# Performance work log

Hardware: AMD Instinct MI355X
Metric: run time of the kernel (lower is better)

## Reference

```python
import jax, jax.numpy as jnp
import numpy as np

N_NODES = 50000
N_EDGES = 800000
FEAT_DIM = 64
NUM_RELS = 8


def setup_inputs() -> dict:
    key = jax.random.key(0)
    k1, k2, k3, k4, k5 = jax.random.split(key, 5)
    features = jax.random.normal(k1, (N_NODES, FEAT_DIM), dtype=jnp.float32)
    # xavier_uniform with relu gain ~= sqrt(2)*sqrt(6/(D+D))
    limit = np.sqrt(2.0) * np.sqrt(6.0 / (FEAT_DIM + FEAT_DIM))
    weight_r = jax.random.uniform(k2, (NUM_RELS, FEAT_DIM, FEAT_DIM), dtype=jnp.float32,
                                  minval=-limit, maxval=limit)
    src = jax.random.randint(k3, (N_EDGES,), 0, N_NODES, dtype=jnp.int64 if jax.config.jax_enable_x64 else jnp.int32)
    dst = jax.random.randint(k4, (N_EDGES,), 0, N_NODES, dtype=src.dtype)
    etype = jax.random.randint(k5, (N_EDGES,), 0, NUM_RELS, dtype=src.dtype)
    return {"features": features, "weight_r": weight_r, "src": src, "dst": dst, "etype": etype}


def reference(features, weight_r, src, dst, etype):
    N, D = features.shape
    c = 0.2
    # in-degree of each destination node (DGL 'deg' node data)
    deg = jax.ops.segment_sum(jnp.ones(dst.shape, dtype=features.dtype), dst, num_segments=N)
    # relation-batched matmul: h @ W_r for every relation, then gather per edge.
    # [R, N, D] = 8*50000*64 floats -- cheap vs. materializing [E, D, D] weights.
    hw = jnp.einsum('nd,rdf->rnf', features, weight_r)
    msg = hw[etype, src] / deg[dst][:, None]          # [E, D]
    M = jax.ops.segment_sum(msg, dst, num_segments=N)  # scatter-sum mailbox reduce
    updated = jax.nn.relu(c * features + (1.0 - c) * M)
    # DGL only applies reduce to nodes that received messages; others keep h.
    return jnp.where((deg > 0)[:, None], updated, features)
```

## Files before the change

kernel.cpp:

```cpp
#include <hip/hip_runtime.h>
#include <hip/hip_bf16.h>

#define N_NODES 50000
#define N_EDGES 800000
#define FEAT 64
#define NRELS 8
#define NBUCK 196
#define EPB 4096
#define NBP 196
#define BCAP 5120
#define FB_BLOCKS 782
#define NPB 32
#define FUSE_BLOCKS 1563

typedef __attribute__((ext_vector_type(8))) short bf16x8;
typedef __attribute__((ext_vector_type(4))) float f32x4;

static __host__ __device__ inline size_t align256(size_t x) { return (x + 255) & ~(size_t)255; }

__device__ inline unsigned short f2b(float f) {
    unsigned u = __builtin_bit_cast(unsigned, f);
    unsigned r = (u + 0x7fffu + ((u >> 16) & 1u)) >> 16;
    return (unsigned short)r;
}
__device__ inline float b2f(unsigned short u) {
    unsigned v = ((unsigned)u) << 16;
    return __builtin_bit_cast(float, v);
}

__global__ void bfill_kernel(const int* __restrict__ dst, const int* __restrict__ srcv,
                             const int* __restrict__ et, const float* __restrict__ W,
                             const float* __restrict__ feat,
                             int* __restrict__ bcnt, int* __restrict__ tmp,
                             unsigned short* __restrict__ WtT,
                             unsigned short* __restrict__ Fb, int E, int N) {
    const int t = threadIdx.x;

    if (blockIdx.x >= NBP) {
        const int fbb = blockIdx.x - NBP;
        if (fbb < 32) {
            int i4 = fbb * 256 + t;
            float4 v = ((const float4*)W)[i4];
            int bse = i4 * 4;
            int f0 = bse & 63;
            int rd = bse >> 6;
            int d  = rd & 63;
            int r  = rd >> 6;
            unsigned short* w0 = WtT + ((size_t)(r * 64 + f0) * 64 + d);
            w0[0 * 64] = f2b(v.x);
            w0[1 * 64] = f2b(v.y);
            w0[2 * 64] = f2b(v.z);
            w0[3 * 64] = f2b(v.w);
        }
        const int node = fbb * 64 + (t >> 2);
        if (node >= N) return;
        const int seg = t & 3;
        const float4* F4 = (const float4*)feat + (size_t)node * 16 + seg * 4;
        float4 v0 = F4[0], v1 = F4[1], v2 = F4[2], v3 = F4[3];
        bf16x8 b0, b1;
        b0[0] = (short)f2b(v0.x); b0[1] = (short)f2b(v0.y);
        b0[2] = (short)f2b(v0.z); b0[3] = (short)f2b(v0.w);
        b0[4] = (short)f2b(v1.x); b0[5] = (short)f2b(v1.y);
        b0[6] = (short)f2b(v1.z); b0[7] = (short)f2b(v1.w);
        b1[0] = (short)f2b(v2.x); b1[1] = (short)f2b(v2.y);
        b1[2] = (short)f2b(v2.z); b1[3] = (short)f2b(v2.w);
        b1[4] = (short)f2b(v3.x); b1[5] = (short)f2b(v3.y);
        b1[6] = (short)f2b(v3.z); b1[7] = (short)f2b(v3.w);
        *(bf16x8*)(Fb + (size_t)node * 64 + seg * 16)     = b0;
        *(bf16x8*)(Fb + (size_t)node * 64 + seg * 16 + 8) = b1;
        return;
    }

    __shared__ int hist[256];
    __shared__ int base[256];
    __shared__ int lcur[256];
    hist[t] = 0; lcur[t] = 0;
    __syncthreads();

    const int4* dst4 = (const int4*)dst;
    const int4* src4 = (const int4*)srcv;
    const int4* et4  = (const int4*)et;
    const int n4 = E >> 2;
    int bk[16], pk[16];
#pragma unroll
    for (int k = 0; k < 4; k++) {
        int i4 = blockIdx.x * 1024 + t + k * 256;
        if (i4 < n4) {
            int4 d = dst4[i4];
            int4 s = src4[i4];
            int4 r = et4[i4];
            const int dd[4] = {d.x, d.y, d.z, d.w};
            const int ss[4] = {s.x, s.y, s.z, s.w};
            const int rr[4] = {r.x, r.y, r.z, r.w};
#pragma unroll
            for (int j = 0; j < 4; j++) {
                int idx = k * 4 + j;
                bk[idx] = dd[j] >> 8;
                pk[idx] = (ss[j] & 0xFFFF) | (rr[j] << 16) | ((dd[j] & 255) << 19);
                atomicAdd(&hist[bk[idx]], 1);
            }
        } else {
#pragma unroll
            for (int j = 0; j < 4; j++) bk[k * 4 + j] = -1;
        }
    }
    __syncthreads();
    if (t < NBUCK && hist[t] > 0)
        base[t] = t * BCAP + atomicAdd(&bcnt[t], hist[t]);
    __syncthreads();
#pragma unroll
    for (int k = 0; k < 16; k++) {
        if (bk[k] >= 0) {
            int r = atomicAdd(&lcur[bk[k]], 1);
            int pos = base[bk[k]] + r;
            if (pos < (bk[k] + 1) * BCAP)
                tmp[pos] = pk[k];
        }
    }
}

__global__ void mid_kernel(const int* __restrict__ bcnt, const int* __restrict__ tmp,
                           int* __restrict__ spk, int* __restrict__ off_s,
                           int* __restrict__ off_e, int N) {
    __shared__ int hist[2048];
    __shared__ int s[256];
    const int t = threadIdx.x;

    const int b = blockIdx.x;
    const int n0 = b * 256;
    const int nn = min(256, N - n0);
    const int s0 = b * BCAP;
    const int s1 = s0 + min(bcnt[b], BCAP);

#pragma unroll
    for (int j = 0; j < 8; j++) hist[t * 8 + j] = 0;
    __syncthreads();
    for (int i = s0 + t; i < s1; i += 1024) {
        int v0 = tmp[i];
        int v1 = (i + 256 < s1) ? tmp[i + 256] : -1;
        int v2 = (i + 512 < s1) ? tmp[i + 512] : -1;
        int v3 = (i + 768 < s1) ? tmp[i + 768] : -1;
        atomicAdd(&hist[(v0 >> 16) & 0x7FF], 1);
        if (v1 >= 0) atomicAdd(&hist[(v1 >> 16) & 0x7FF], 1);
        if (v2 >= 0) atomicAdd(&hist[(v2 >> 16) & 0x7FF], 1);
        if (v3 >= 0) atomicAdd(&hist[(v3 >> 16) & 0x7FF], 1);
    }
    __syncthreads();
    int loc[8], st[8], T = 0;
#pragma unroll
    for (int j = 0; j < 8; j++) loc[j] = hist[t * 8 + j];
#pragma unroll
    for (int j = 0; j < 8; j++) { st[j] = T; T += loc[j]; }
    s[t] = T;
    __syncthreads();
    for (int o = 1; o < 256; o <<= 1) {
        int u = (t >= o) ? s[t - o] : 0;
        __syncthreads();
        s[t] += u;
        __syncthreads();
    }
    const int base = s0 + s[t] - T;
    if (t < nn) {
        off_s[n0 + t] = base;
        off_e[n0 + t] = base + T;
    }
#pragma unroll
    for (int j = 0; j < 8; j++) hist[t * 8 + j] = base + st[j];
    __syncthreads();
    for (int i = s0 + t; i < s1; i += 1024) {
        int v0 = tmp[i];
        int v1 = (i + 256 < s1) ? tmp[i + 256] : -1;
        int v2 = (i + 512 < s1) ? tmp[i + 512] : -1;
        int v3 = (i + 768 < s1) ? tmp[i + 768] : -1;
        int p0 = atomicAdd(&hist[(v0 >> 16) & 0x7FF], 1);
        spk[p0] = v0;
        if (v1 >= 0) { int p1 = atomicAdd(&hist[(v1 >> 16) & 0x7FF], 1); spk[p1] = v1; }
        if (v2 >= 0) { int p2 = atomicAdd(&hist[(v2 >> 16) & 0x7FF], 1); spk[p2] = v2; }
        if (v3 >= 0) { int p3 = atomicAdd(&hist[(v3 >> 16) & 0x7FF], 1); spk[p3] = v3; }
    }
}

__global__ __launch_bounds__(256, 4) void fuse_kernel(
    const int* __restrict__ off_s, const int* __restrict__ off_e,
    const int* __restrict__ spk, const unsigned short* __restrict__ Fb,
    const unsigned short* __restrict__ WtT, const float* __restrict__ feat,
    float* __restrict__ out, int N) {
    __shared__ unsigned short Sb[NRELS][NPB][64];
    const int t = threadIdx.x;
    const int n0 = blockIdx.x * NPB;
    const int nn = min(NPB, N - n0);

    {
        f32x4 z = {0.f, 0.f, 0.f, 0.f};
        f32x4* zp = (f32x4*)&Sb[0][0][0];
#pragma unroll
        for (int i = 0; i < 8; i++) zp[t + 256 * i] = z;
    }
    __syncthreads();

    const int gid = t >> 3, q = t & 7;
    const int lanebase = (t & 63) & ~7;
    if (gid < nn) {
        const int gn = n0 + gid;
        const int b = off_s[gn], e = off_e[gn];
        const int swz = (q ^ (gid & 7)) * 8;
        unsigned short* srow = &Sb[0][0][0] + (size_t)gid * 64 + swz;
        float a[8] = {0.f, 0.f, 0.f, 0.f, 0.f, 0.f, 0.f, 0.f};
        int curR = -1;

        auto flushS = [&](int rel) {
            bf16x8 v;
#pragma unroll
            for (int k = 0; k < 8; k++) v[k] = (short)f2b(a[k]);
            *(bf16x8*)(srow + (size_t)rel * (NPB * 64)) = v;
        };

        int pks0 = (b + q      < e) ? spk[b + q]      : -1;
        int pks1 = (b + q + 8  < e) ? spk[b + q + 8]  : -1;
        int pks2 = (b + q + 16 < e) ? spk[b + q + 16] : -1;
        int pks3 = (b + q + 24 < e) ? spk[b + q + 24] : -1;

        int pkj[32];
#pragma unroll
        for (int j = 0; j < 8; j++) pkj[j]      = __shfl(pks0, lanebase | j);
#pragma unroll
        for (int j = 0; j < 8; j++) pkj[8 + j]  = __shfl(pks1, lanebase | j);
#pragma unroll
        for (int j = 0; j < 8; j++) pkj[16 + j] = __shfl(pks2, lanebase | j);
#pragma unroll
        for (int j = 0; j < 8; j++) pkj[24 + j] = __shfl(pks3, lanebase | j);

        bf16x8 u[8];
#pragma unroll
        for (int j = 0; j < 8; j++) {
            u[j] = (bf16x8){0, 0, 0, 0, 0, 0, 0, 0};
            if (pkj[j] >= 0)
                u[j] = *(const bf16x8*)(Fb + (size_t)(pkj[j] & 0xFFFF) * 64 + q * 8);
        }
#pragma unroll
        for (int j = 0; j < 32; j++) {
            bf16x8 uu = u[j & 7];
            if (j + 8 < 32) {
                if (pkj[j + 8] >= 0)
                    u[j & 7] = *(const bf16x8*)(Fb + (size_t)(pkj[j + 8] & 0xFFFF) * 64 + q * 8);
            }
            if (pkj[j] >= 0) {
                int rel = (pkj[j] >> 16) & 7;
                if (rel != curR) {
                    if (curR >= 0) flushS(curR);
                    curR = rel;
#pragma unroll
                    for (int k = 0; k < 8; k++) a[k] = 0.f;
                }
#pragma unroll
                for (int k = 0; k < 8; k++) a[k] += b2f((unsigned short)uu[k]);
            }
        }
        for (int i = b + 32; i < e; i++) {
            int pk = spk[i];
            bf16x8 uu = *(const bf16x8*)(Fb + (size_t)(pk & 0xFFFF) * 64 + q * 8);
            int rel = (pk >> 16) & 7;
            if (rel != curR) {
                if (curR >= 0) flushS(curR);
                curR = rel;
#pragma unroll
                for (int k = 0; k < 8; k++) a[k] = 0.f;
            }
#pragma unroll
            for (int k = 0; k < 8; k++) a[k] += b2f((unsigned short)uu[k]);
        }
        if (curR >= 0) flushS(curR);
    }
    __syncthreads();

    const int w = t >> 6, l = t & 63, col = l & 15, quad = l >> 4;
    f32x4 acc0 = {0.f, 0.f, 0.f, 0.f}, acc1 = {0.f, 0.f, 0.f, 0.f};
    const int sw0 = (quad ^ (col & 7)) * 8;
    const int sw1 = ((quad + 4) ^ (col & 7)) * 8;
#pragma unroll
    for (int r = 0; r < NRELS; r++) {
        const unsigned short* wp = WtT + (size_t)r * 4096 + ((w * 16 + col) * 64 + quad * 8);
        bf16x8 b0 = *(const bf16x8*)wp;
        bf16x8 b1 = *(const bf16x8*)(wp + 32);
        const unsigned short* Sr = &Sb[0][0][0] + (size_t)r * (NPB * 64);
        bf16x8 a0 = *(const bf16x8*)&Sr[col * 64 + sw0];
        bf16x8 a1 = *(const bf16x8*)&Sr[col * 64 + sw1];
        bf16x8 c0 = *(const bf16x8*)&Sr[(16 + col) * 64 + sw0];
        bf16x8 c1 = *(const bf16x8*)&Sr[(16 + col) * 64 + sw1];
        acc0 = __builtin_amdgcn_mfma_f32_16x16x32_bf16(a0, b0, acc0, 0, 0, 0);
        acc0 = __builtin_amdgcn_mfma_f32_16x16x32_bf16(a1, b1, acc0, 0, 0, 0);
        acc1 = __builtin_amdgcn_mfma_f32_16x16x32_bf16(c0, b0, acc1, 0, 0, 0);
        acc1 = __builtin_amdgcn_mfma_f32_16x16x32_bf16(c1, b1, acc1, 0, 0, 0);
    }
    __syncthreads();

    float* C = (float*)&Sb[0][0][0];
#pragma unroll
    for (int i = 0; i < 4; i++) {
        C[(quad * 4 + i) * 72 + w * 16 + col]        = acc0[i];
        C[(16 + quad * 4 + i) * 72 + w * 16 + col]   = acc1[i];
    }
    __syncthreads();

    {
        const int n = t >> 3;
        if (n < nn) {
            const int gn = n0 + n;
            const int f0 = (t & 7) * 8;
            const int deg = off_e[gn] - off_s[gn];
            float4 m0 = *(const float4*)&C[n * 72 + f0];
            float4 m1 = *(const float4*)&C[n * 72 + f0 + 4];
            const float4* fp = (const float4*)feat + (size_t)gn * 16 + (f0 >> 2);
            float4 h0 = fp[0], h1 = fp[1];
            float4 r0, r1;
            if (deg > 0) {
                float inv = 0.8f / (float)deg;
                r0.x = fmaxf(0.2f * h0.x + m0.x * inv, 0.f);
                r0.y = fmaxf(0.2f * h0.y + m0.y * inv, 0.f);
                r0.z = fmaxf(0.2f * h0.z + m0.z * inv, 0.f);
                r0.w = fmaxf(0.2f * h0.w + m0.w * inv, 0.f);
                r1.x = fmaxf(0.2f * h1.x + m1.x * inv, 0.f);
                r1.y = fmaxf(0.2f * h1.y + m1.y * inv, 0.f);
                r1.z = fmaxf(0.2f * h1.z + m1.z * inv, 0.f);
                r1.w = fmaxf(0.2f * h1.w + m1.w * inv, 0.f);
            } else {
                r0 = h0; r1 = h1;
            }
            float4* op = (float4*)out + (size_t)gn * 16 + (f0 >> 2);
            op[0] = r0;
            op[1] = r1;
        }
    }
}

__global__ void degf_kernel(const int* __restrict__ dst, float* __restrict__ deg, int E) {
    int e = blockIdx.x * blockDim.x + threadIdx.x;
    if (e < E) atomicAdd(deg + dst[e], 1.0f);
}

__global__ void otf_kernel(const int* __restrict__ src, const int* __restrict__ dst,
                           const int* __restrict__ et, const float* __restrict__ feat,
                           const float* __restrict__ W, float* __restrict__ out, int E) {
    int wid = (blockIdx.x * blockDim.x + threadIdx.x) >> 6;
    int l = threadIdx.x & 63;
    if (wid >= E) return;
    int s = src[wid], dd = dst[wid], r = et[wid];
    float fv = feat[(size_t)s * 64 + l];
    const float* Wr = W + (size_t)r * 4096;
    float acc = 0.f;
#pragma unroll
    for (int d = 0; d < 64; d++) {
        float a = __shfl(fv, d);
        acc += a * Wr[d * 64 + l];
    }
    atomicAdd(out + (size_t)dd * 64 + l, acc);
}

__global__ void final_kernel(const float* __restrict__ feat, const float* __restrict__ deg,
                             float* __restrict__ out, int N) {
    int i = blockIdx.x * blockDim.x + threadIdx.x;
    if (i >= N * 16) return;
    int n = i >> 4;
    float d = deg[n];
    float4 f = ((const float4*)feat)[i];
    float4 m = ((float4*)out)[i];
    float4 res;
    if (d > 0.f) {
        float inv = 0.8f / d;
        res.x = fmaxf(0.2f * f.x + m.x * inv, 0.f);
        res.y = fmaxf(0.2f * f.y + m.y * inv, 0.f);
        res.z = fmaxf(0.2f * f.z + m.z * inv, 0.f);
        res.w = fmaxf(0.2f * f.w + m.w * inv, 0.f);
    } else {
        res = f;
    }
    ((float4*)out)[i] = res;
}

extern "C" void kernel_launch(void* const* d_in, const int* in_sizes, int n_in,
                              void* d_out, int out_size, void* d_ws, size_t ws_size,
                              hipStream_t stream) {
    const float* feat = (const float*)d_in[0];
    const float* W    = (const float*)d_in[1];
    const int*   src  = (const int*)d_in[2];
    const int*   dst  = (const int*)d_in[3];
    const int*   et   = (const int*)d_in[4];
    float* out = (float*)d_out;

    const int N = N_NODES, E = N_EDGES;

    char* p = (char*)d_ws;
    int* bcnt  = (int*)p;  p += align256((size_t)NBUCK * 4);
    int* off_s = (int*)p;  p += align256((size_t)N * 4);
    int* off_e = (int*)p;  p += align256((size_t)N * 4);
    int* tmp   = (int*)p;  p += align256((size_t)NBUCK * BCAP * 4);
    int* spk   = (int*)p;  p += align256((size_t)NBUCK * BCAP * 4);
    unsigned short* WtT = (unsigned short*)p;
    p += align256((size_t)NRELS * FEAT * FEAT * 2);
    unsigned short* Fb = (unsigned short*)p;
    p += align256((size_t)N * FEAT * 2);
    size_t need_full = (size_t)(p - (char*)d_ws);

    if (ws_size >= need_full) {
        hipMemsetAsync(bcnt, 0, (size_t)NBUCK * 4, stream);
        bfill_kernel<<<NBP + FB_BLOCKS, 256, 0, stream>>>(dst, src, et, W, feat,
                                                          bcnt, tmp, WtT, Fb, E, N);
        mid_kernel<<<NBUCK, 256, 0, stream>>>(bcnt, tmp, spk, off_s, off_e, N);
        fuse_kernel<<<FUSE_BLOCKS, 256, 0, stream>>>(off_s, off_e, spk, Fb, WtT,
                                                     feat, out, N);
    } else {
        float* deg = (float*)d_ws;
        hipMemsetAsync(out, 0, (size_t)N * FEAT * 4, stream);
        hipMemsetAsync(deg, 0, (size_t)N * 4, stream);
        degf_kernel<<<(E + 255) / 256, 256, 0, stream>>>(dst, deg, E);
        otf_kernel<<<(E + 3) / 4, 256, 0, stream>>>(src, dst, et, feat, W, out, E);
        final_kernel<<<(N * 16 + 255) / 256, 256, 0, stream>>>(feat, deg, out, N);
    }
}
```

Before: 123.4 us.

## Use finer 128-node buckets and prefetch feature/offset loads in fused kernel

The bucket sort now groups edges by dst>>7 into 391 buckets of capacity 2816 instead of 196 buckets of 256 nodes. The mid kernel's per-node histogram shrinks accordingly, giving smaller shared arrays and more blocks. The fuse kernel loads offsets and self-features before the LDS zeroing so their latency is hidden. It also shuffles edge packs lazily per tier and exits early for short edge lists. Risks: bucket overflow with a smaller capacity, and the mid/fill launch grid sizes (not shown) must match the new bucket count.

```diff
diff --git a/kernel.cpp b/kernel.cpp
--- a/kernel.cpp
+++ b/kernel.cpp
@@ -5,10 +5,9 @@
 #define N_EDGES 800000
 #define FEAT 64
 #define NRELS 8
-#define NBUCK 196
-#define EPB 4096
+#define NBUCK 391
 #define NBP 196
-#define BCAP 5120
+#define BCAP 2816
 #define FB_BLOCKS 782
 #define NPB 32
 #define FUSE_BLOCKS 1563
@@ -71,10 +70,10 @@
         return;
     }
 
-    __shared__ int hist[256];
-    __shared__ int base[256];
-    __shared__ int lcur[256];
-    hist[t] = 0; lcur[t] = 0;
+    __shared__ int hist[392];
+    __shared__ int base[392];
+    __shared__ int lcur[392];
+    for (int j = t; j < 392; j += 256) { hist[j] = 0; lcur[j] = 0; }
     __syncthreads();
 
     const int4* dst4 = (const int4*)dst;
@@ -95,8 +94,8 @@
 #pragma unroll
             for (int j = 0; j < 4; j++) {
                 int idx = k * 4 + j;
-                bk[idx] = dd[j] >> 8;
-                pk[idx] = (ss[j] & 0xFFFF) | (rr[j] << 16) | ((dd[j] & 255) << 19);
+                bk[idx] = dd[j] >> 7;
+                pk[idx] = (ss[j] & 0xFFFF) | (rr[j] << 16) | ((dd[j] & 127) << 19);
                 atomicAdd(&hist[bk[idx]], 1);
             }
         } else {
@@ -105,8 +104,9 @@
         }
     }
     __syncthreads();
-    if (t < NBUCK && hist[t] > 0)
-        base[t] = t * BCAP + atomicAdd(&bcnt[t], hist[t]);
+    for (int j = t; j < NBUCK; j += 256)
+        if (hist[j] > 0)
+            base[j] = j * BCAP + atomicAdd(&bcnt[j], hist[j]);
     __syncthreads();
 #pragma unroll
     for (int k = 0; k < 16; k++) {
@@ -122,35 +122,34 @@
 __global__ void mid_kernel(const int* __restrict__ bcnt, const int* __restrict__ tmp,
                            int* __restrict__ spk, int* __restrict__ off_s,
                            int* __restrict__ off_e, int N) {
-    __shared__ int hist[2048];
+    __shared__ int hist[1024];
     __shared__ int s[256];
     const int t = threadIdx.x;
 
     const int b = blockIdx.x;
-    const int n0 = b * 256;
-    const int nn = min(256, N - n0);
+    const int n0 = b * 128;
+    const int nn = min(128, N - n0);
     const int s0 = b * BCAP;
     const int s1 = s0 + min(bcnt[b], BCAP);
 
-#pragma unroll
-    for (int j = 0; j < 8; j++) hist[t * 8 + j] = 0;
+    *(int4*)&hist[t * 4] = make_int4(0, 0, 0, 0);
     __syncthreads();
     for (int i = s0 + t; i < s1; i += 1024) {
         int v0 = tmp[i];
         int v1 = (i + 256 < s1) ? tmp[i + 256] : -1;
         int v2 = (i + 512 < s1) ? tmp[i + 512] : -1;
         int v3 = (i + 768 < s1) ? tmp[i + 768] : -1;
-        atomicAdd(&hist[(v0 >> 16) & 0x7FF], 1);
-        if (v1 >= 0) atomicAdd(&hist[(v1 >> 16) & 0x7FF], 1);
-        if (v2 >= 0) atomicAdd(&hist[(v2 >> 16) & 0x7FF], 1);
-        if (v3 >= 0) atomicAdd(&hist[(v3 >> 16) & 0x7FF], 1);
-    }
-    __syncthreads();
-    int loc[8], st[8], T = 0;
-#pragma unroll
-    for (int j = 0; j < 8; j++) loc[j] = hist[t * 8 + j];
-#pragma unroll
-    for (int j = 0; j < 8; j++) { st[j] = T; T += loc[j]; }
+        atomicAdd(&hist[(v0 >> 16) & 1023], 1);
+        if (v1 >= 0) atomicAdd(&hist[(v1 >> 16) & 1023], 1);
+        if (v2 >= 0) atomicAdd(&hist[(v2 >> 16) & 1023], 1);
+        if (v3 >= 0) atomicAdd(&hist[(v3 >> 16) & 1023], 1);
+    }
+    __syncthreads();
+    int loc[4], st4[4], T = 0;
+#pragma unroll
+    for (int j = 0; j < 4; j++) loc[j] = hist[t * 4 + j];
+#pragma unroll
+    for (int j = 0; j < 4; j++) { st4[j] = T; T += loc[j]; }
     s[t] = T;
     __syncthreads();
     for (int o = 1; o < 256; o <<= 1) {
@@ -159,24 +158,27 @@
         s[t] += u;
         __syncthreads();
     }
-    const int base = s0 + s[t] - T;
-    if (t < nn) {
-        off_s[n0 + t] = base;
-        off_e[n0 + t] = base + T;
-    }
-#pragma unroll
-    for (int j = 0; j < 8; j++) hist[t * 8 + j] = base + st[j];
+    const int ex = s[t] - T;
+    {
+        const int n = t >> 1;
+        if (n < nn) {
+            if ((t & 1) == 0) off_s[n0 + n] = s0 + ex;
+            else              off_e[n0 + n] = s0 + ex + T;
+        }
+    }
+#pragma unroll
+    for (int j = 0; j < 4; j++) hist[t * 4 + j] = s0 + ex + st4[j];
     __syncthreads();
     for (int i = s0 + t; i < s1; i += 1024) {
         int v0 = tmp[i];
         int v1 = (i + 256 < s1) ? tmp[i + 256] : -1;
         int v2 = (i + 512 < s1) ? tmp[i + 512] : -1;
         int v3 = (i + 768 < s1) ? tmp[i + 768] : -1;
-        int p0 = atomicAdd(&hist[(v0 >> 16) & 0x7FF], 1);
+        int p0 = atomicAdd(&hist[(v0 >> 16) & 1023], 1);
         spk[p0] = v0;
-        if (v1 >= 0) { int p1 = atomicAdd(&hist[(v1 >> 16) & 0x7FF], 1); spk[p1] = v1; }
-        if (v2 >= 0) { int p2 = atomicAdd(&hist[(v2 >> 16) & 0x7FF], 1); spk[p2] = v2; }
-        if (v3 >= 0) { int p3 = atomicAdd(&hist[(v3 >> 16) & 0x7FF], 1); spk[p3] = v3; }
+        if (v1 >= 0) { int p1 = atomicAdd(&hist[(v1 >> 16) & 1023], 1); spk[p1] = v1; }
+        if (v2 >= 0) { int p2 = atomicAdd(&hist[(v2 >> 16) & 1023], 1); spk[p2] = v2; }
+        if (v3 >= 0) { int p3 = atomicAdd(&hist[(v3 >> 16) & 1023], 1); spk[p3] = v3; }
     }
 }
 
@@ -189,6 +191,23 @@
     const int t = threadIdx.x;
     const int n0 = blockIdx.x * NPB;
     const int nn = min(NPB, N - n0);
+    const int gid = t >> 3, q = t & 7;
+    const int lanebase = (t & 63) & ~7;
+
+    int b = 0, e = 0;
+    if (gid < nn) {
+        const int gn = n0 + gid;
+        b = off_s[gn];
+        e = off_e[gn];
+    }
+
+    float4 h0e = make_float4(0.f, 0.f, 0.f, 0.f), h1e = h0e;
+    const int ef0 = q * 8;
+    if (gid < nn) {
+        const float4* fp = (const float4*)feat + (size_t)(n0 + gid) * 16 + (ef0 >> 2);
+        h0e = fp[0];
+        h1e = fp[1];
+    }
 
     {
         f32x4 z = {0.f, 0.f, 0.f, 0.f};
@@ -198,11 +217,7 @@
     }
     __syncthreads();
 
-    const int gid = t >> 3, q = t & 7;
-    const int lanebase = (t & 63) & ~7;
-    if (gid < nn) {
-        const int gn = n0 + gid;
-        const int b = off_s[gn], e = off_e[gn];
+    if (gid < nn && b < e) {
         const int swz = (q ^ (gid & 7)) * 8;
         unsigned short* srow = &Sb[0][0][0] + (size_t)gid * 64 + swz;
         float a[8] = {0.f, 0.f, 0.f, 0.f, 0.f, 0.f, 0.f, 0.f};
@@ -215,45 +230,47 @@
             *(bf16x8*)(srow + (size_t)rel * (NPB * 64)) = v;
         };
 
-        int pks0 = (b + q      < e) ? spk[b + q]      : -1;
-        int pks1 = (b + q + 8  < e) ? spk[b + q + 8]  : -1;
-        int pks2 = (b + q + 16 < e) ? spk[b + q + 16] : -1;
-        int pks3 = (b + q + 24 < e) ? spk[b + q + 24] : -1;
-
-        int pkj[32];
-#pragma unroll
-        for (int j = 0; j < 8; j++) pkj[j]      = __shfl(pks0, lanebase | j);
-#pragma unroll
-        for (int j = 0; j < 8; j++) pkj[8 + j]  = __shfl(pks1, lanebase | j);
-#pragma unroll
-        for (int j = 0; j < 8; j++) pkj[16 + j] = __shfl(pks2, lanebase | j);
-#pragma unroll
-        for (int j = 0; j < 8; j++) pkj[24 + j] = __shfl(pks3, lanebase | j);
+        int pks[4];
+#pragma unroll
+        for (int k = 0; k < 4; k++)
+            pks[k] = (b + q + 8 * k < e) ? spk[b + q + 8 * k] : -1;
 
         bf16x8 u[8];
+        int pkv[8];
 #pragma unroll
         for (int j = 0; j < 8; j++) {
+            int pk = __shfl(pks[0], lanebase | j);
+            pkv[j] = pk;
             u[j] = (bf16x8){0, 0, 0, 0, 0, 0, 0, 0};
-            if (pkj[j] >= 0)
-                u[j] = *(const bf16x8*)(Fb + (size_t)(pkj[j] & 0xFFFF) * 64 + q * 8);
-        }
-#pragma unroll
-        for (int j = 0; j < 32; j++) {
-            bf16x8 uu = u[j & 7];
-            if (j + 8 < 32) {
-                if (pkj[j + 8] >= 0)
-                    u[j & 7] = *(const bf16x8*)(Fb + (size_t)(pkj[j + 8] & 0xFFFF) * 64 + q * 8);
-            }
-            if (pkj[j] >= 0) {
-                int rel = (pkj[j] >> 16) & 7;
-                if (rel != curR) {
-                    if (curR >= 0) flushS(curR);
-                    curR = rel;
-#pragma unroll
-                    for (int k = 0; k < 8; k++) a[k] = 0.f;
+            if (pk >= 0)
+                u[j] = *(const bf16x8*)(Fb + (size_t)(pk & 0xFFFF) * 64 + q * 8);
+        }
+#pragma unroll
+        for (int tier = 0; tier < 4; tier++) {
+            if (b + tier * 8 >= e) break;
+#pragma unroll
+            for (int jj = 0; jj < 8; jj++) {
+                const int j = tier * 8 + jj;
+                bf16x8 uu = u[jj];
+                int pk = pkv[jj];
+                if (tier < 3) {
+                    int pkn = __shfl(pks[(j + 8) >> 3], lanebase | jj);
+                    pkv[jj] = pkn;
+                    if (pkn >= 0)
+                        u[jj] = *(const bf16x8*)(Fb + (size_t)(pkn & 0xFFFF) * 64 + q * 8);
                 }
-#pragma unroll
-                for (int k = 0; k < 8; k++) a[k] += b2f((unsigned short)uu[k]);
+                if (pk >= 0) {
+                    int rel = (pk >> 16) & 7;
+                    if (rel != curR) {
+                        if (curR >= 0) flushS(curR);
+                        curR = rel;
+#pragma unroll
+                        for (int k = 0; k < 8; k++) a[k] = b2f((unsigned short)uu[k]);
+                    } else {
+#pragma unroll
+                        for (int k = 0; k < 8; k++) a[k] += b2f((unsigned short)uu[k]);
+                    }
+                }
             }
         }
         for (int i = b + 32; i < e; i++) {
@@ -264,10 +281,11 @@
                 if (curR >= 0) flushS(curR);
                 curR = rel;
 #pragma unroll
-                for (int k = 0; k < 8; k++) a[k] = 0.f;
+                for (int k = 0; k < 8; k++) a[k] = b2f((unsigned short)uu[k]);
+            } else {
+#pragma unroll
+                for (int k = 0; k < 8; k++) a[k] += b2f((unsigned short)uu[k]);
             }
-#pragma unroll
-            for (int k = 0; k < 8; k++) a[k] += b2f((unsigned short)uu[k]);
         }
         if (curR >= 0) flushS(curR);
     }
@@ -302,34 +320,28 @@
     }
     __syncthreads();
 
-    {
-        const int n = t >> 3;
-        if (n < nn) {
-            const int gn = n0 + n;
-            const int f0 = (t & 7) * 8;
-            const int deg = off_e[gn] - off_s[gn];
-            float4 m0 = *(const float4*)&C[n * 72 + f0];
-            float4 m1 = *(const float4*)&C[n * 72 + f0 + 4];
-            const float4* fp = (const float4*)feat + (size_t)gn * 16 + (f0 >> 2);
-            float4 h0 = fp[0], h1 = fp[1];
-            float4 r0, r1;
-            if (deg > 0) {
-                float inv = 0.8f / (float)deg;
-                r0.x = fmaxf(0.2f * h0.x + m0.x * inv, 0.f);
-                r0.y = fmaxf(0.2f * h0.y + m0.y * inv, 0.f);
-                r0.z = fmaxf(0.2f * h0.z + m0.z * inv, 0.f);
-                r0.w = fmaxf(0.2f * h0.w + m0.w * inv, 0.f);
-                r1.x = fmaxf(0.2f * h1.x + m1.x * inv, 0.f);
-                r1.y = fmaxf(0.2f * h1.y + m1.y * inv, 0.f);
-                r1.z = fmaxf(0.2f * h1.z + m1.z * inv, 0.f);
-                r1.w = fmaxf(0.2f * h1.w + m1.w * inv, 0.f);
-            } else {
-                r0 = h0; r1 = h1;
-            }
-            float4* op = (float4*)out + (size_t)gn * 16 + (f0 >> 2);
-            op[0] = r0;
-            op[1] = r1;
-        }
+    if (gid < nn) {
+        const int gn = n0 + gid;
+        const int deg = e - b;
+        float4 m0 = *(const float4*)&C[gid * 72 + ef0];
+        float4 m1 = *(const float4*)&C[gid * 72 + ef0 + 4];
+        float4 r0, r1;
+        if (deg > 0) {
+            float inv = 0.8f / (float)deg;
+            r0.x = fmaxf(0.2f * h0e.x + m0.x * inv, 0.f);
+            r0.y = fmaxf(0.2f * h0e.y + m0.y * inv, 0.f);
+            r0.z = fmaxf(0.2f * h0e.z + m0.z * inv, 0.f);
+            r0.w = fmaxf(0.2f * h0e.w + m0.w * inv, 0.f);
+            r1.x = fmaxf(0.2f * h1e.x + m1.x * inv, 0.f);
+            r1.y = fmaxf(0.2f * h1e.y + m1.y * inv, 0.f);
+            r1.z = fmaxf(0.2f * h1e.z + m1.z * inv, 0.f);
+            r1.w = fmaxf(0.2f * h1e.w + m1.w * inv, 0.f);
+        } else {
+            r0 = h0e; r1 = h1e;
+        }
+        float4* op = (float4*)out + (size_t)gn * 16 + (ef0 >> 2);
+        op[0] = r0;
+        op[1] = r1;
     }
 }
 
```

Measured after the change: 129.9 us. 5.3% more time.
